# Kernel tuning notes

Hardware: AMD Instinct MI355X
Metric: run time of the kernel (lower is better)

The kernel has to match this reference:

```python
import jax, jax.numpy as jnp
import numpy as np

B, N, C = 16, 1024, 768            # N = window_size**2 = 32*32
NUM_HEADS, BANK = 12, 256
HEAD_DIM = C // NUM_HEADS
LN_EPS = 1e-5


def setup_inputs() -> dict:
    key = jax.random.key(0)
    ks = jax.random.split(key, 9)
    s = 0.02
    return {
        "x": jax.random.normal(ks[0], (B, N, C), dtype=jnp.float32),
        "qkv_w": jax.random.normal(ks[1], (3 * C, C), dtype=jnp.float32) * s,
        "qkv_b": jnp.zeros((3 * C,), dtype=jnp.float32),
        "proj_w": jax.random.normal(ks[2], (C, C), dtype=jnp.float32) * s,
        "proj_b": jnp.zeros((C,), dtype=jnp.float32),
        "norm_w": jnp.ones((C,), dtype=jnp.float32),
        "norm_b": jnp.zeros((C,), dtype=jnp.float32),
        "bank_k": jax.random.normal(ks[3], (BANK, C), dtype=jnp.float32) * s,
        "bank_v": jax.random.normal(ks[4], (BANK, C), dtype=jnp.float32) * s,
    }


def _split_heads_bank(bank, b):
    # (BANK, C) -> broadcast to (b, BANK, C) -> (b, H, BANK, D)
    t = jnp.broadcast_to(bank, (b,) + bank.shape)
    return t.reshape(b, BANK, NUM_HEADS, HEAD_DIM).transpose(0, 2, 1, 3)


def reference(x, qkv_w, qkv_b, proj_w, proj_b, norm_w, norm_b, bank_k, bank_v):
    b, n, c = x.shape
    h, d = NUM_HEADS, HEAD_DIM
    # QKV projection: (b, n, 3c) -> (3, b, h, n, d)
    qkv = (jnp.einsum("bnc,fc->bnf", x, qkv_w) + qkv_b)
    qkv = qkv.reshape(b, n, 3, h, d).transpose(2, 0, 3, 1, 4)
    q, k, v = qkv[0], qkv[1], qkv[2]
    # Memory-bank read + concat onto KV
    k_full = jnp.concatenate([k, _split_heads_bank(bank_k, b)], axis=2)  # (b,h,n+BANK,d)
    v_full = jnp.concatenate([v, _split_heads_bank(bank_v, b)], axis=2)
    # SDPA (dropout_p = 0.0)
    scores = jnp.einsum("bhnd,bhmd->bhnm", q, k_full) / jnp.sqrt(jnp.asarray(d, x.dtype))
    attn = jax.nn.softmax(scores, axis=-1)
    out = jnp.einsum("bhnm,bhmd->bhnd", attn, v_full)
    out = out.transpose(0, 2, 1, 3).reshape(b, n, c)
    # Bank write value: LayerNorm(proj(out))  (side effect in torch; returned here)
    p = jnp.einsum("bnc,oc->bno", out, proj_w) + proj_b
    mu = jnp.mean(p, axis=-1, keepdims=True)
    var = jnp.mean(jnp.square(p - mu), axis=-1, keepdims=True)
    bank_update = (p - mu) * jax.lax.rsqrt(var + LN_EPS) * norm_w + norm_b
    return out, bank_update
```

## Files before the change

### kernel.cpp

```cpp
#include <hip/hip_runtime.h>

typedef __attribute__((ext_vector_type(8))) short short8;
typedef __attribute__((ext_vector_type(4))) float float4_t;
typedef unsigned short u16;

#define K_DIM 768

__device__ __forceinline__ u16 f2bf(float f) {
  union { float f; unsigned u; } v; v.f = f;
  unsigned r = v.u + 0x7FFFu + ((v.u >> 16) & 1u);
  return (u16)(r >> 16);
}

__device__ __forceinline__ u16 f2bf_trunc(float f) {
  union { float f; unsigned u; } v; v.f = f;
  return (u16)(v.u >> 16);
}

__device__ __forceinline__ void gload16(const void* g, void* l) {
  __builtin_amdgcn_global_load_lds(
      (__attribute__((address_space(1))) void*)g,
      (__attribute__((address_space(3))) void*)l, 16, 0, 0);
}

__global__ __launch_bounds__(256) void cvt_all_kernel(
    const float* __restrict__ x, const float* __restrict__ qw,
    const float* __restrict__ pw, const float* __restrict__ bkf,
    const float* __restrict__ bvf,
    u16* __restrict__ xbf, u16* __restrict__ qwbf, u16* __restrict__ pwbf,
    u16* __restrict__ bk, u16* __restrict__ bvt) {
  const int blk = blockIdx.x;
  if (blk < 14592) {
    int i = blk * 256 + threadIdx.x;
    const float* src; u16* dst;
    if (i < 3145728)      { src = x;  dst = xbf; }
    else if (i < 3588096) { src = qw; dst = qwbf; i -= 3145728; }
    else                  { src = pw; dst = pwbf; i -= 3588096; }
    float4 v = ((const float4*)src)[i];
    union { u16 h[4]; unsigned long long ll; } o;
    o.h[0] = f2bf(v.x); o.h[1] = f2bf(v.y); o.h[2] = f2bf(v.z); o.h[3] = f2bf(v.w);
    ((unsigned long long*)dst)[i] = o.ll;
  } else {
    int idx = (blk - 14592) * 256 + threadIdx.x;
    int m = idx / 768;
    int c = idx - m * 768;
    int h = c >> 6, d = c & 63;
    bk[(h * 256 + m) * 64 + d] = f2bf(bkf[idx]);
    bvt[(h * 64 + d) * 256 + m] = f2bf(bvf[idx]);
  }
}

template <int MODE>
__global__ __launch_bounds__(256) void gemm128(
    const u16* __restrict__ A, const u16* __restrict__ Bw,
    const float* __restrict__ bias,
    u16* __restrict__ q_ws, u16* __restrict__ k_ws, u16* __restrict__ vt_ws,
    float* __restrict__ p_out) {
  __shared__ u16 As[2][128 * 32];
  __shared__ u16 Bs[2][128 * 32];
  const int tid = threadIdx.x;
  const int w = tid >> 6, lane = tid & 63;
  const int l15 = lane & 15, quad = lane >> 4;
  const int wm = w >> 1, wn = w & 1;

  constexpr int NBN = (MODE == 0) ? 18 : 6;
  const int bid = blockIdx.x;
  const int xcd = bid & 7, local = bid >> 3;
  const int bm = xcd * 16 + local / NBN;
  const int bn = local % NBN;

  float4_t acc[4][4];
#pragma unroll
  for (int i = 0; i < 4; i++)
#pragma unroll
    for (int j = 0; j < 4; j++) acc[i][j] = (float4_t){0.f, 0.f, 0.f, 0.f};

  auto stage = [&](int buf, int kt) {
#pragma unroll
    for (int r = 0; r < 2; r++) {
      const int off = (w * 2 + r) * 1024 + lane * 16;
      const int row = off >> 6;
      const int grp = (off & 63) >> 4;
      const int lcol = (grp ^ (row & 3)) * 8;
      gload16(A + (size_t)(bm * 128 + row) * K_DIM + kt + lcol, (char*)As[buf] + off);
      gload16(Bw + (size_t)(bn * 128 + row) * K_DIM + kt + lcol, (char*)Bs[buf] + off);
    }
  };

  stage(0, 0);
  __syncthreads();
  int cur = 0;
  for (int kt = 0; kt < K_DIM; kt += 32) {
    if (kt + 32 < K_DIM) stage(cur ^ 1, kt + 32);
    short8 af[4], bfr[4];
#pragma unroll
    for (int mt = 0; mt < 4; mt++) {
      const int row = wm * 64 + mt * 16 + l15;
      af[mt] = *(const short8*)(As[cur] + row * 32 + (quad ^ (row & 3)) * 8);
    }
#pragma unroll
    for (int nt = 0; nt < 4; nt++) {
      const int row = wn * 64 + nt * 16 + l15;
      bfr[nt] = *(const short8*)(Bs[cur] + row * 32 + (quad ^ (row & 3)) * 8);
    }
#pragma unroll
    for (int mt = 0; mt < 4; mt++)
#pragma unroll
      for (int nt = 0; nt < 4; nt++)
        acc[mt][nt] = __builtin_amdgcn_mfma_f32_16x16x32_bf16(af[mt], bfr[nt], acc[mt][nt], 0, 0, 0);
    __syncthreads();
    cur ^= 1;
  }

  const float QS = 0.18033688011112042f;
#pragma unroll
  for (int mt = 0; mt < 4; mt++) {
#pragma unroll
    for (int nt = 0; nt < 4; nt++) {
      const int row0 = bm * 128 + wm * 64 + mt * 16 + quad * 4;
      const int f = bn * 128 + wn * 64 + nt * 16 + l15;
      const float bv = bias[f];
      if (MODE == 0) {
        const int which = f / 768;
        const int rem = f - which * 768;
        const int h = rem >> 6, d = rem & 63;
#pragma unroll
        for (int r2 = 0; r2 < 4; r2++) {
          float v = acc[mt][nt][r2] + bv;
          const int i = row0 + r2;
          const int bb = i >> 10, n = i & 1023;
          const size_t bhh = (size_t)(bb * 12 + h);
          if (which == 0)      q_ws[(bhh * 1024 + n) * 64 + d] = f2bf(v * QS);
          else if (which == 1) k_ws[(bhh * 1024 + n) * 64 + d] = f2bf(v);
          else                 vt_ws[(bhh * 64 + d) * 1024 + n] = f2bf(v);
        }
      } else {
#pragma unroll
        for (int r2 = 0; r2 < 4; r2++) {
          const int i = row0 + r2;
          p_out[(size_t)i * 768 + f] = acc[mt][nt][r2] + bv;
        }
      }
    }
  }
}

__global__ __launch_bounds__(256) void fa_kernel(
    const u16* __restrict__ qws, const u16* __restrict__ kws,
    const u16* __restrict__ vtws, const u16* __restrict__ bk,
    const u16* __restrict__ bvt,
    float* __restrict__ out, u16* __restrict__ obf) {
  __shared__ u16 smem[8192];
  u16* Ks  = smem;
  u16* Vts = smem + 4096;

  const int tid = threadIdx.x;
  const int w = tid >> 6, lane = tid & 63;
  const int l15 = lane & 15, quad = lane >> 4;
  u16* Psw = smem + w * 2048;
  const int bh = blockIdx.x;
  const int b = bh / 12, h = bh - b * 12;
  const int q0 = blockIdx.y * 128 + w * 32;

  short8 qf[2][2];
  {
    const u16* qb = qws + ((size_t)bh * 1024 + q0) * 64;
#pragma unroll
    for (int rt = 0; rt < 2; rt++)
#pragma unroll
      for (int c = 0; c < 2; c++)
        qf[rt][c] = *(const short8*)(qb + (rt * 16 + l15) * 64 + c * 32 + quad * 8);
  }

  const short ONE = (short)0x3F80;
  const short8 onesf = (short8){ONE, ONE, ONE, ONE, ONE, ONE, ONE, ONE};

  float4_t O[2][4];
  float4_t lacc[2];
#pragma unroll
  for (int rt = 0; rt < 2; rt++) {
#pragma unroll
    for (int dt = 0; dt < 4; dt++) O[rt][dt] = (float4_t){0.f, 0.f, 0.f, 0.f};
    lacc[rt] = (float4_t){0.f, 0.f, 0.f, 0.f};
  }

  for (int t = 0; t < 20; t++) {
    const int mb = t * 64;
    __syncthreads();
#pragma unroll
    for (int r = 0; r < 2; r++) {
      const int off = (w * 2 + r) * 1024 + lane * 16;
      const int row = off >> 7;
      const int grp = (off & 127) >> 4;
      const int lcol = (grp ^ (row & 7)) * 8;
      const u16* g = (mb < 1024)
          ? kws + ((size_t)bh * 1024 + mb + row) * 64 + lcol
          : bk + ((size_t)h * 256 + (mb - 1024) + row) * 64 + lcol;
      gload16(g, (char*)Ks + off);
      const u16* g2 = (mb < 1024)
          ? vtws + ((size_t)bh * 64 + row) * 1024 + mb + lcol
          : bvt + ((size_t)h * 64 + row) * 256 + (mb - 1024) + lcol;
      gload16(g2, (char*)Vts + off);
    }
    __syncthreads();

    short8 kf[4][2];
#pragma unroll
    for (int ct = 0; ct < 4; ct++)
#pragma unroll
      for (int c = 0; c < 2; c++) {
        const int row = ct * 16 + l15;
        kf[ct][c] = *(const short8*)(Ks + row * 64 + ((c * 4 + quad) ^ (row & 7)) * 8);
      }

    float4_t S[2][4];
#pragma unroll
    for (int rt = 0; rt < 2; rt++)
#pragma unroll
      for (int ct = 0; ct < 4; ct++) {
        float4_t z = (float4_t){0.f, 0.f, 0.f, 0.f};
        z = __builtin_amdgcn_mfma_f32_16x16x32_bf16(qf[rt][0], kf[ct][0], z, 0, 0, 0);
        S[rt][ct] = __builtin_amdgcn_mfma_f32_16x16x32_bf16(qf[rt][1], kf[ct][1], z, 0, 0, 0);
      }

    short8 vf[4][2];
#pragma unroll
    for (int dt = 0; dt < 4; dt++)
#pragma unroll
      for (int c = 0; c < 2; c++) {
        const int row = dt * 16 + l15;
        vf[dt][c] = *(const short8*)(Vts + row * 64 + ((c * 4 + quad) ^ (row & 7)) * 8);
      }

    __syncthreads();

#pragma unroll
    for (int rt = 0; rt < 2; rt++) {
#pragma unroll
      for (int ct = 0; ct < 4; ct++) {
        const int colg = ct * 2 + (l15 >> 3);
#pragma unroll
        for (int r = 0; r < 4; r++) {
          const float p = __builtin_amdgcn_exp2f(S[rt][ct][r]);
          const int q = rt * 16 + quad * 4 + r;
          Psw[q * 64 + (colg ^ (q & 7)) * 8 + (l15 & 7)] = f2bf_trunc(p);
        }
      }
    }

#pragma unroll
    for (int rt = 0; rt < 2; rt++)
#pragma unroll
      for (int c = 0; c < 2; c++) {
        const int qrow = rt * 16 + l15;
        const short8 pf = *(const short8*)(&Psw[qrow * 64 + (((c * 4 + quad) ^ (qrow & 7)) * 8)]);
#pragma unroll
        for (int dt = 0; dt < 4; dt++)
          O[rt][dt] = __builtin_amdgcn_mfma_f32_16x16x32_bf16(pf, vf[dt][c], O[rt][dt], 0, 0, 0);
        lacc[rt] = __builtin_amdgcn_mfma_f32_16x16x32_bf16(pf, onesf, lacc[rt], 0, 0, 0);
      }
  }

#pragma unroll
  for (int rt = 0; rt < 2; rt++) {
    float rl[4];
#pragma unroll
    for (int r = 0; r < 4; r++) rl[r] = 1.f / lacc[rt][r];
#pragma unroll
    for (int dt = 0; dt < 4; dt++)
#pragma unroll
      for (int r = 0; r < 4; r++) {
        const float v = O[rt][dt][r] * rl[r];
        const int n = q0 + rt * 16 + quad * 4 + r;
        const int d = dt * 16 + l15;
        const size_t idx = ((size_t)b * 1024 + n) * 768 + h * 64 + d;
        out[idx] = v;
        obf[idx] = f2bf(v);
      }
  }
}

__global__ __launch_bounds__(256) void ln_kernel(float* __restrict__ p,
                                                 const float* __restrict__ nw,
                                                 const float* __restrict__ nb) {
  __shared__ float red[2][4];
  const int row = blockIdx.x, tid = threadIdx.x;
  float* pr = p + (size_t)row * 768;
  const float x0 = pr[tid], x1 = pr[tid + 256], x2 = pr[tid + 512];
  float s = x0 + x1 + x2;
  float sq = x0 * x0 + x1 * x1 + x2 * x2;
#pragma unroll
  for (int m = 1; m < 64; m <<= 1) {
    s += __shfl_xor(s, m, 64);
    sq += __shfl_xor(sq, m, 64);
  }
  const int w = tid >> 6;
  if ((tid & 63) == 0) { red[0][w] = s; red[1][w] = sq; }
  __syncthreads();
  s = red[0][0] + red[0][1] + red[0][2] + red[0][3];
  sq = red[1][0] + red[1][1] + red[1][2] + red[1][3];
  const float mean = s * (1.0f / 768.0f);
  const float var = sq * (1.0f / 768.0f) - mean * mean;
  const float rstd = rsqrtf(var + 1e-5f);
  pr[tid]       = (x0 - mean) * rstd * nw[tid]       + nb[tid];
  pr[tid + 256] = (x1 - mean) * rstd * nw[tid + 256] + nb[tid + 256];
  pr[tid + 512] = (x2 - mean) * rstd * nw[tid + 512] + nb[tid + 512];
}

extern "C" void kernel_launch(void* const* d_in, const int* in_sizes, int n_in,
                              void* d_out, int out_size, void* d_ws, size_t ws_size,
                              hipStream_t stream) {
  (void)in_sizes; (void)n_in; (void)out_size; (void)ws_size;
  const float* x      = (const float*)d_in[0];
  const float* qkv_w  = (const float*)d_in[1];
  const float* qkv_b  = (const float*)d_in[2];
  const float* proj_w = (const float*)d_in[3];
  const float* proj_b = (const float*)d_in[4];
  const float* norm_w = (const float*)d_in[5];
  const float* norm_b = (const float*)d_in[6];
  const float* bank_k = (const float*)d_in[7];
  const float* bank_v = (const float*)d_in[8];

  char* ws = (char*)d_ws;
  u16* xbf   = (u16*)(ws + 0);
  u16* obf   = (u16*)(ws + 0);
  u16* qwbf  = (u16*)(ws + 25165824);
  u16* pwbf  = (u16*)(ws + 28704768);
  u16* bkbf  = (u16*)(ws + 29884416);
  u16* bvtbf = (u16*)(ws + 30277632);
  u16* q_ws  = (u16*)(ws + 30670848);
  u16* k_ws  = (u16*)(ws + 55836672);
  u16* vt_ws = (u16*)(ws + 81002496);

  float* out0  = (float*)d_out;
  float* p_out = out0 + 12582912;

  cvt_all_kernel<<<15360, 256, 0, stream>>>(x, qkv_w, proj_w, bank_k, bank_v,
                                            xbf, qwbf, pwbf, bkbf, bvtbf);

  gemm128<0><<<dim3(2304), 256, 0, stream>>>(xbf, qwbf, qkv_b, q_ws, k_ws, vt_ws, nullptr);
  fa_kernel<<<dim3(192, 8), 256, 0, stream>>>(q_ws, k_ws, vt_ws, bkbf, bvtbf, out0, obf);
  gemm128<1><<<dim3(768), 256, 0, stream>>>(obf, pwbf, proj_b, nullptr, nullptr, nullptr, p_out);
  ln_kernel<<<16384, 256, 0, stream>>>(p_out, norm_w, norm_b);
}
```

Before: 429.0 us.

## Deepen GEMM K-tile to 64 and double-buffer K/V loads in attention

The GEMM now stages 64-wide K slices (12 iterations instead of 24) with a precomputed swizzled offset table and an 8-way XOR swizzle, which halves the barrier count per tile and doubles the MFMA work per sync. The attention kernel gains a second LDS buffer so the next K/V tile is prefetched while the current one is computed. Its __syncthreads calls are replaced with explicit waitcnt plus s_barrier and sched_barrier fences. This doubles LDS use in both kernels, which may lower occupancy, and the hand-placed waits must be exactly right for the P scratch that now aliases the current K buffer.

New measurement: 400.7 us. -6.6%, faster.

```diff
diff --git a/kernel.cpp b/kernel.cpp
--- a/kernel.cpp
+++ b/kernel.cpp
@@ -51,13 +51,13 @@
 }
 
 template <int MODE>
-__global__ __launch_bounds__(256) void gemm128(
+__global__ __launch_bounds__(256) void gemm128b(
     const u16* __restrict__ A, const u16* __restrict__ Bw,
     const float* __restrict__ bias,
     u16* __restrict__ q_ws, u16* __restrict__ k_ws, u16* __restrict__ vt_ws,
     float* __restrict__ p_out) {
-  __shared__ u16 As[2][128 * 32];
-  __shared__ u16 Bs[2][128 * 32];
+  __shared__ u16 As[2][8192];
+  __shared__ u16 Bs[2][8192];
   const int tid = threadIdx.x;
   const int w = tid >> 6, lane = tid & 63;
   const int l15 = lane & 15, quad = lane >> 4;
@@ -69,47 +69,68 @@
   const int bm = xcd * 16 + local / NBN;
   const int bn = local % NBN;
 
+  int soff[4], loff[4];
+#pragma unroll
+  for (int r = 0; r < 4; r++) {
+    const int off = r * 4096 + tid * 16;
+    const int row = off >> 7;
+    const int grp = (off & 127) >> 4;
+    soff[r] = row * K_DIM + (grp ^ (row & 7)) * 8;
+    loff[r] = off;
+  }
+  const u16* Abase = A + (size_t)bm * 128 * K_DIM;
+  const u16* Bbase = Bw + (size_t)bn * 128 * K_DIM;
+
+  auto stg = [&](const u16* g0, u16* l0, int kt) {
+#pragma unroll
+    for (int r = 0; r < 4; r++)
+      gload16(g0 + soff[r] + kt, (char*)l0 + loff[r]);
+  };
+
+  const int ab0 = l15 * 128 + ((quad ^ (l15 & 7)) << 4);
+  const int ab1 = l15 * 128 + (((4 + quad) ^ (l15 & 7)) << 4);
+
   float4_t acc[4][4];
 #pragma unroll
   for (int i = 0; i < 4; i++)
 #pragma unroll
     for (int j = 0; j < 4; j++) acc[i][j] = (float4_t){0.f, 0.f, 0.f, 0.f};
 
-  auto stage = [&](int buf, int kt) {
-#pragma unroll
-    for (int r = 0; r < 2; r++) {
-      const int off = (w * 2 + r) * 1024 + lane * 16;
-      const int row = off >> 6;
-      const int grp = (off & 63) >> 4;
-      const int lcol = (grp ^ (row & 3)) * 8;
-      gload16(A + (size_t)(bm * 128 + row) * K_DIM + kt + lcol, (char*)As[buf] + off);
-      gload16(Bw + (size_t)(bn * 128 + row) * K_DIM + kt + lcol, (char*)Bs[buf] + off);
-    }
-  };
-
-  stage(0, 0);
+  stg(Abase, As[0], 0);
+  stg(Bbase, Bs[0], 0);
   __syncthreads();
-  int cur = 0;
-  for (int kt = 0; kt < K_DIM; kt += 32) {
-    if (kt + 32 < K_DIM) stage(cur ^ 1, kt + 32);
-    short8 af[4], bfr[4];
+
+  int buf = 0;
+#pragma unroll 1
+  for (int t = 0; t < 12; t++) {
+    if (t < 11) {
+      stg(Abase, As[buf ^ 1], (t + 1) * 64);
+      stg(Bbase, Bs[buf ^ 1], (t + 1) * 64);
+    }
+    short8 af[4][2], bfr[4][2];
 #pragma unroll
     for (int mt = 0; mt < 4; mt++) {
-      const int row = wm * 64 + mt * 16 + l15;
-      af[mt] = *(const short8*)(As[cur] + row * 32 + (quad ^ (row & 3)) * 8);
+      const char* p = (const char*)As[buf] + ((wm * 64 + mt * 16) << 7);
+      af[mt][0] = *(const short8*)(p + ab0);
+      af[mt][1] = *(const short8*)(p + ab1);
     }
 #pragma unroll
     for (int nt = 0; nt < 4; nt++) {
-      const int row = wn * 64 + nt * 16 + l15;
-      bfr[nt] = *(const short8*)(Bs[cur] + row * 32 + (quad ^ (row & 3)) * 8);
+      const char* p = (const char*)Bs[buf] + ((wn * 64 + nt * 16) << 7);
+      bfr[nt][0] = *(const short8*)(p + ab0);
+      bfr[nt][1] = *(const short8*)(p + ab1);
     }
 #pragma unroll
     for (int mt = 0; mt < 4; mt++)
 #pragma unroll
-      for (int nt = 0; nt < 4; nt++)
-        acc[mt][nt] = __builtin_amdgcn_mfma_f32_16x16x32_bf16(af[mt], bfr[nt], acc[mt][nt], 0, 0, 0);
+      for (int nt = 0; nt < 4; nt++) {
+        acc[mt][nt] = __builtin_amdgcn_mfma_f32_16x16x32_bf16(
+            af[mt][0], bfr[nt][0], acc[mt][nt], 0, 0, 0);
+        acc[mt][nt] = __builtin_amdgcn_mfma_f32_16x16x32_bf16(
+            af[mt][1], bfr[nt][1], acc[mt][nt], 0, 0, 0);
+      }
     __syncthreads();
-    cur ^= 1;
+    buf ^= 1;
   }
 
   const float QS = 0.18033688011112042f;
@@ -150,14 +171,11 @@
     const u16* __restrict__ vtws, const u16* __restrict__ bk,
     const u16* __restrict__ bvt,
     float* __restrict__ out, u16* __restrict__ obf) {
-  __shared__ u16 smem[8192];
-  u16* Ks  = smem;
-  u16* Vts = smem + 4096;
+  __shared__ u16 smem[2][8192];
 
   const int tid = threadIdx.x;
   const int w = tid >> 6, lane = tid & 63;
   const int l15 = lane & 15, quad = lane >> 4;
-  u16* Psw = smem + w * 2048;
   const int bh = blockIdx.x;
   const int b = bh / 12, h = bh - b * 12;
   const int q0 = blockIdx.y * 128 + w * 32;
@@ -184,9 +202,10 @@
     lacc[rt] = (float4_t){0.f, 0.f, 0.f, 0.f};
   }
 
-  for (int t = 0; t < 20; t++) {
-    const int mb = t * 64;
-    __syncthreads();
+  auto stage = [&](int tt, int buf) {
+    const int mb = tt * 64;
+    u16* Ksb = &smem[buf][0];
+    u16* Vtb = &smem[buf][4096];
 #pragma unroll
     for (int r = 0; r < 2; r++) {
       const int off = (w * 2 + r) * 1024 + lane * 16;
@@ -196,13 +215,28 @@
       const u16* g = (mb < 1024)
           ? kws + ((size_t)bh * 1024 + mb + row) * 64 + lcol
           : bk + ((size_t)h * 256 + (mb - 1024) + row) * 64 + lcol;
-      gload16(g, (char*)Ks + off);
+      gload16(g, (char*)Ksb + off);
       const u16* g2 = (mb < 1024)
           ? vtws + ((size_t)bh * 64 + row) * 1024 + mb + lcol
           : bvt + ((size_t)h * 64 + row) * 256 + (mb - 1024) + lcol;
-      gload16(g2, (char*)Vts + off);
-    }
-    __syncthreads();
+      gload16(g2, (char*)Vtb + off);
+    }
+  };
+
+  stage(0, 0);
+  __builtin_amdgcn_sched_barrier(0);
+  asm volatile("s_waitcnt vmcnt(0)" ::: "memory");
+  __builtin_amdgcn_s_barrier();
+  __builtin_amdgcn_sched_barrier(0);
+
+#pragma unroll 1
+  for (int t = 0; t < 20; t++) {
+    const int cur = t & 1;
+    if (t < 19) stage(t + 1, cur ^ 1);
+
+    const u16* Ks  = &smem[cur][0];
+    const u16* Vts = &smem[cur][4096];
+    u16* Psw = &smem[cur][0] + w * 2048;
 
     short8 kf[4][2];
 #pragma unroll
@@ -232,7 +266,10 @@
         vf[dt][c] = *(const short8*)(Vts + row * 64 + ((c * 4 + quad) ^ (row & 7)) * 8);
       }
 
-    __syncthreads();
+    __builtin_amdgcn_sched_barrier(0);
+    asm volatile("s_waitcnt lgkmcnt(0)" ::: "memory");
+    __builtin_amdgcn_s_barrier();
+    __builtin_amdgcn_sched_barrier(0);
 
 #pragma unroll
     for (int rt = 0; rt < 2; rt++) {
@@ -259,6 +296,11 @@
           O[rt][dt] = __builtin_amdgcn_mfma_f32_16x16x32_bf16(pf, vf[dt][c], O[rt][dt], 0, 0, 0);
         lacc[rt] = __builtin_amdgcn_mfma_f32_16x16x32_bf16(pf, onesf, lacc[rt], 0, 0, 0);
       }
+
+    __builtin_amdgcn_sched_barrier(0);
+    asm volatile("s_waitcnt vmcnt(0) lgkmcnt(0)" ::: "memory");
+    __builtin_amdgcn_s_barrier();
+    __builtin_amdgcn_sched_barrier(0);
   }
 
 #pragma unroll
@@ -338,8 +380,8 @@
   cvt_all_kernel<<<15360, 256, 0, stream>>>(x, qkv_w, proj_w, bank_k, bank_v,
                                             xbf, qwbf, pwbf, bkbf, bvtbf);
 
-  gemm128<0><<<dim3(2304), 256, 0, stream>>>(xbf, qwbf, qkv_b, q_ws, k_ws, vt_ws, nullptr);
+  gemm128b<0><<<dim3(2304), 256, 0, stream>>>(xbf, qwbf, qkv_b, q_ws, k_ws, vt_ws, nullptr);
   fa_kernel<<<dim3(192, 8), 256, 0, stream>>>(q_ws, k_ws, vt_ws, bkbf, bvtbf, out0, obf);
-  gemm128<1><<<dim3(768), 256, 0, stream>>>(obf, pwbf, proj_b, nullptr, nullptr, nullptr, p_out);
+  gemm128b<1><<<dim3(768), 256, 0, stream>>>(obf, pwbf, proj_b, nullptr, nullptr, nullptr, p_out);
   ln_kernel<<<16384, 256, 0, stream>>>(p_out, norm_w, norm_b);
 }
```
